# Kernel optimization log

Hardware: AMD Instinct MI355X
Metric: run time of the kernel (lower is better)

Reference implementation:

```python
import jax, jax.numpy as jnp
import numpy as np

S = 4096
DMODEL = 1024
DK = 128

def setup_inputs() -> dict:
    key = jax.random.key(0)
    ks = jax.random.split(key, 7)
    X = jax.random.normal(ks[0], (S, DMODEL), dtype=jnp.float32)
    # nn.Linear(dmodel, dk): weight [dk, dmodel], bias [dk]
    sc = 1.0 / np.sqrt(DMODEL)
    Wq = jax.random.uniform(ks[1], (DK, DMODEL), jnp.float32, -sc, sc)
    bq = jax.random.uniform(ks[2], (DK,), jnp.float32, -sc, sc)
    Wk = jax.random.uniform(ks[3], (DK, DMODEL), jnp.float32, -sc, sc)
    bk = jax.random.uniform(ks[4], (DK,), jnp.float32, -sc, sc)
    Wv = jax.random.uniform(ks[5], (DK, DMODEL), jnp.float32, -sc, sc)
    bv = jax.random.uniform(ks[6], (DK,), jnp.float32, -sc, sc)
    return {"X": X, "Wq": Wq, "bq": bq, "Wk": Wk, "bk": bk, "Wv": Wv, "bv": bv}

def reference(X, Wq, bq, Wk, bk, Wv, bv):
    # QKV projections: [S, dk]
    Q = X @ Wq.T + bq
    K = X @ Wk.T + bk
    V = X @ Wv.T + bv
    scale = 1.0 / jnp.sqrt(jnp.asarray(DK, X.dtype))
    scores = (Q @ K.T) * scale  # [S, S]
    s = X.shape[0]
    causal = jnp.tril(jnp.ones((s, s), dtype=bool))  # True = keep
    scores = jnp.where(causal, scores, -jnp.inf)
    A = jax.nn.softmax(scores, axis=-1)  # dropout p=0 -> identity
    return A @ V  # [S, dk]
```

## Files before the change

### kernel.cpp

```cpp
#include <hip/hip_runtime.h>
#include <hip/hip_bf16.h>

#define S 4096
#define DMODEL 1024
#define DK 128
#define NB_ATTN 2112

typedef __attribute__((ext_vector_type(8))) short  short8;
typedef __attribute__((ext_vector_type(4))) float  f32x4;
typedef __attribute__((ext_vector_type(4))) unsigned short u16x4;

__device__ __forceinline__ unsigned short f2bf(float f) {
    return __builtin_bit_cast(unsigned short, __float2bfloat16(f));
}

__device__ __forceinline__ short8 cvt8(float4 a, float4 b) {
    short8 v;
    v[0] = (short)f2bf(a.x); v[1] = (short)f2bf(a.y);
    v[2] = (short)f2bf(a.z); v[3] = (short)f2bf(a.w);
    v[4] = (short)f2bf(b.x); v[5] = (short)f2bf(b.y);
    v[6] = (short)f2bf(b.z); v[7] = (short)f2bf(b.w);
    return v;
}

__global__ __launch_bounds__(256) void cvt_kernel(
    const float* __restrict__ X,
    const float* __restrict__ Wq, const float* __restrict__ Wk,
    const float* __restrict__ Wv,
    unsigned short* __restrict__ Xb, unsigned short* __restrict__ Wb)
{
    const int i = blockIdx.x * 256 + threadIdx.x;
    const float* __restrict__ src;
    unsigned short* __restrict__ dst;
    size_t off;
    if (i < 524288) {
        src = X; dst = Xb; off = (size_t)i * 8;
    } else {
        const int j   = i - 524288;
        const int sel = j >> 14, jj = j & 16383;
        src = sel == 0 ? Wq : sel == 1 ? Wk : Wv;
        dst = Wb + (size_t)sel * DK * DMODEL;
        off = (size_t)jj * 8;
    }
    const float4 a = *(const float4*)(src + off);
    const float4 b = *(const float4*)(src + off + 4);
    *(short8*)(dst + off) = cvt8(a, b);
}

__global__ __launch_bounds__(128) void proj_gemm(
    const unsigned short* __restrict__ Xb, const unsigned short* __restrict__ Wb,
    const float* __restrict__ bq, const float* __restrict__ bk,
    const float* __restrict__ bv,
    unsigned short* __restrict__ Qb, unsigned short* __restrict__ Kb,
    unsigned short* __restrict__ Vt)
{
    const int sel = blockIdx.y;
    const float* __restrict__ bias = sel == 0 ? bq : sel == 1 ? bk : bv;
    const unsigned short* __restrict__ wbase = Wb + (size_t)sel * DK * DMODEL;

    const int tid = threadIdx.x, w = tid >> 6, lane = tid & 63;
    const int li = lane & 15, gl = lane >> 4;
    const int r0 = blockIdx.x * 16;
    const int n0 = w * 64;

    f32x4 acc[4];
    #pragma unroll
    for (int j = 0; j < 4; ++j)
        #pragma unroll
        for (int r = 0; r < 4; ++r) acc[j][r] = 0.f;

    const unsigned short* ap  = &Xb[(size_t)(r0 + li) * DMODEL + 8 * gl];
    const unsigned short* bp0 = &wbase[(size_t)(n0 + li) * DMODEL + 8 * gl];
    const unsigned short* bp1 = bp0 + (size_t)16 * DMODEL;
    const unsigned short* bp2 = bp0 + (size_t)32 * DMODEL;
    const unsigned short* bp3 = bp0 + (size_t)48 * DMODEL;

    #pragma unroll 4
    for (int k0 = 0; k0 < DMODEL; k0 += 32) {
        const short8 a  = *(const short8*)(ap + k0);
        const short8 b0 = *(const short8*)(bp0 + k0);
        const short8 b1 = *(const short8*)(bp1 + k0);
        const short8 b2 = *(const short8*)(bp2 + k0);
        const short8 b3 = *(const short8*)(bp3 + k0);
        acc[0] = __builtin_amdgcn_mfma_f32_16x16x32_bf16(a, b0, acc[0], 0, 0, 0);
        acc[1] = __builtin_amdgcn_mfma_f32_16x16x32_bf16(a, b1, acc[1], 0, 0, 0);
        acc[2] = __builtin_amdgcn_mfma_f32_16x16x32_bf16(a, b2, acc[2], 0, 0, 0);
        acc[3] = __builtin_amdgcn_mfma_f32_16x16x32_bf16(a, b3, acc[3], 0, 0, 0);
    }

    if (sel < 2) {
        unsigned short* __restrict__ Out = sel == 0 ? Qb : Kb;
        #pragma unroll
        for (int j = 0; j < 4; ++j)
            #pragma unroll
            for (int r = 0; r < 4; ++r) {
                const int row = r0 + 4 * gl + r;
                const int col = n0 + 16 * j + li;
                Out[(size_t)row * DK + col] = f2bf(acc[j][r] + bias[col]);
            }
    } else {
        #pragma unroll
        for (int j = 0; j < 4; ++j) {
            const int col = n0 + 16 * j + li;
            const float bb = bias[col];
            u16x4 wv;
            #pragma unroll
            for (int r = 0; r < 4; ++r) wv[r] = f2bf(acc[j][r] + bb);
            *(u16x4*)&Vt[(size_t)col * S + r0 + 4 * gl] = wv;
        }
    }
}

__global__ __launch_bounds__(64) void attn_mfma(
    const unsigned short* __restrict__ Qb,
    const unsigned short* __restrict__ Kb,
    const unsigned short* __restrict__ Vt,
    float* __restrict__ OP, float* __restrict__ ML)
{
    const int b = (NB_ATTN - 1) - (int)blockIdx.x;
    int j = 1;
    while (2 * (j + 1) * j <= b) ++j;
    const int off = b - 2 * j * (j - 1);
    const int t   = 4 * (j - 1) + off / j;
    const int c   = off % j;
    const int kstart = 128 * c;
    const int kend   = min(128 * (c + 1), 32 * t + 32);

    const int lane = threadIdx.x, li = lane & 15, gl = lane >> 4;

    __shared__ unsigned short Pl[32][40];

    short8 aq[2][4];
    #pragma unroll
    for (int qs = 0; qs < 2; ++qs)
        #pragma unroll
        for (int s = 0; s < 4; ++s)
            aq[qs][s] = *(const short8*)
                &Qb[(size_t)(32 * t + 16 * qs + li) * DK + 32 * s + 8 * gl];

    f32x4 accv[2][8];
    #pragma unroll
    for (int qs = 0; qs < 2; ++qs)
        #pragma unroll
        for (int n = 0; n < 8; ++n)
            #pragma unroll
            for (int r = 0; r < 4; ++r) accv[qs][n][r] = 0.f;

    float mr[2] = {-1e30f, -1e30f}, lr[2] = {0.f, 0.f};
    const float scale = 0.08838834764831845f;

    short8 bkc[2][4], bkn[2][4];
    #pragma unroll
    for (int kt = 0; kt < 2; ++kt)
        #pragma unroll
        for (int s = 0; s < 4; ++s)
            bkc[kt][s] = *(const short8*)
                &Kb[(size_t)(kstart + 16 * kt + li) * DK + 32 * s + 8 * gl];

    for (int kb = kstart; kb < kend; kb += 32) {
        short8 bv[8];
        #pragma unroll
        for (int n = 0; n < 8; ++n)
            bv[n] = *(const short8*)&Vt[(size_t)(16 * n + li) * S + kb + 8 * gl];

        f32x4 sc[2][2];
        #pragma unroll
        for (int qs = 0; qs < 2; ++qs)
            #pragma unroll
            for (int kt = 0; kt < 2; ++kt)
                #pragma unroll
                for (int r = 0; r < 4; ++r) sc[qs][kt][r] = 0.f;
        __builtin_amdgcn_s_setprio(1);
        #pragma unroll
        for (int qs = 0; qs < 2; ++qs)
            #pragma unroll
            for (int kt = 0; kt < 2; ++kt)
                #pragma unroll
                for (int s = 0; s < 4; ++s)
                    sc[qs][kt] = __builtin_amdgcn_mfma_f32_16x16x32_bf16(
                        bkc[kt][s], aq[qs][s], sc[qs][kt], 0, 0, 0);
        __builtin_amdgcn_s_setprio(0);

        const int kn = (kb + 32 < kend) ? kb + 32 : kb;
        #pragma unroll
        for (int kt = 0; kt < 2; ++kt)
            #pragma unroll
            for (int s = 0; s < 4; ++s)
                bkn[kt][s] = *(const short8*)
                    &Kb[(size_t)(kn + 16 * kt + li) * DK + 32 * s + 8 * gl];

        #pragma unroll
        for (int qs = 0; qs < 2; ++qs) {
            const int q = 32 * t + 16 * qs + li;
            #pragma unroll
            for (int kt = 0; kt < 2; ++kt)
                #pragma unroll
                for (int r = 0; r < 4; ++r) {
                    const int key = kb + 16 * kt + 4 * gl + r;
                    sc[qs][kt][r] = (key > q) ? -1e30f : sc[qs][kt][r] * scale;
                }
        }

        float tm[2];
        #pragma unroll
        for (int qs = 0; qs < 2; ++qs) {
            float v = fmaxf(fmaxf(fmaxf(sc[qs][0][0], sc[qs][0][1]),
                                  fmaxf(sc[qs][0][2], sc[qs][0][3])),
                            fmaxf(fmaxf(sc[qs][1][0], sc[qs][1][1]),
                                  fmaxf(sc[qs][1][2], sc[qs][1][3])));
            v = fmaxf(v, __shfl_xor(v, 16));
            v = fmaxf(v, __shfl_xor(v, 32));
            tm[qs] = v;
        }

        const int need = (tm[0] > mr[0] + 6.f) | (tm[1] > mr[1] + 6.f);
        if (__any(need)) {
            float corr[2];
            #pragma unroll
            for (int qs = 0; qs < 2; ++qs) {
                const float mnew = fmaxf(mr[qs], tm[qs]);
                corr[qs] = __expf(mr[qs] - mnew);
                lr[qs] *= corr[qs];
                mr[qs]  = mnew;
            }
            #pragma unroll
            for (int qs = 0; qs < 2; ++qs)
                #pragma unroll
                for (int r = 0; r < 4; ++r) {
                    const float cr = __shfl(corr[qs], 4 * gl + r);
                    #pragma unroll
                    for (int n = 0; n < 8; ++n) accv[qs][n][r] *= cr;
                }
        }

        #pragma unroll
        for (int qs = 0; qs < 2; ++qs) {
            float ps = 0.f;
            #pragma unroll
            for (int kt = 0; kt < 2; ++kt)
                #pragma unroll
                for (int r = 0; r < 4; ++r) {
                    const float p = __expf(sc[qs][kt][r] - mr[qs]);
                    sc[qs][kt][r] = p;
                    ps += p;
                }
            ps += __shfl_xor(ps, 16);
            ps += __shfl_xor(ps, 32);
            lr[qs] += ps;
        }

        #pragma unroll
        for (int qs = 0; qs < 2; ++qs)
            #pragma unroll
            for (int kt = 0; kt < 2; ++kt) {
                u16x4 wv;
                #pragma unroll
                for (int r = 0; r < 4; ++r) wv[r] = f2bf(sc[qs][kt][r]);
                *(u16x4*)&Pl[16 * qs + li][16 * kt + 4 * gl] = wv;
            }
        const short8 pa0 = *(const short8*)&Pl[li][8 * gl];
        const short8 pa1 = *(const short8*)&Pl[16 + li][8 * gl];

        __builtin_amdgcn_s_setprio(1);
        #pragma unroll
        for (int n = 0; n < 8; ++n) {
            accv[0][n] = __builtin_amdgcn_mfma_f32_16x16x32_bf16(pa0, bv[n], accv[0][n], 0, 0, 0);
            accv[1][n] = __builtin_amdgcn_mfma_f32_16x16x32_bf16(pa1, bv[n], accv[1][n], 0, 0, 0);
        }
        __builtin_amdgcn_s_setprio(0);

        #pragma unroll
        for (int kt = 0; kt < 2; ++kt)
            #pragma unroll
            for (int s = 0; s < 4; ++s) bkc[kt][s] = bkn[kt][s];
    }

    #pragma unroll
    for (int qs = 0; qs < 2; ++qs)
        #pragma unroll
        for (int n = 0; n < 8; ++n)
            #pragma unroll
            for (int r = 0; r < 4; ++r)
                OP[((size_t)b * 32 + 16 * qs + 4 * gl + r) * DK + 16 * n + li]
                    = accv[qs][n][r];
    if (gl == 0) {
        #pragma unroll
        for (int qs = 0; qs < 2; ++qs) {
            ML[((size_t)b * 32 + 16 * qs + li) * 2 + 0] = mr[qs];
            ML[((size_t)b * 32 + 16 * qs + li) * 2 + 1] = lr[qs];
        }
    }
}

__global__ __launch_bounds__(DK) void merge_kernel(
    const float* __restrict__ OP, const float* __restrict__ ML,
    float* __restrict__ out)
{
    const int row = blockIdx.x, dv = threadIdx.x;
    const int t  = row >> 5, rl = row & 31;
    const int j  = (t >> 2) + 1;
    const int base = 2 * j * (j - 1) + (t & 3) * j;

    float M = -1e30f;
    for (int c = 0; c < j; ++c)
        M = fmaxf(M, ML[((size_t)(base + c) * 32 + rl) * 2]);
    float L = 0.f, o = 0.f;
    for (int c = 0; c < j; ++c) {
        const float mc = ML[((size_t)(base + c) * 32 + rl) * 2 + 0];
        const float lc = ML[((size_t)(base + c) * 32 + rl) * 2 + 1];
        const float wgt = __expf(mc - M);
        L += lc * wgt;
        o += wgt * OP[((size_t)(base + c) * 32 + rl) * DK + dv];
    }
    out[(size_t)row * DK + dv] = o / L;
}

extern "C" void kernel_launch(void* const* d_in, const int* in_sizes, int n_in,
                              void* d_out, int out_size, void* d_ws, size_t ws_size,
                              hipStream_t stream)
{
    (void)in_sizes; (void)n_in; (void)out_size; (void)ws_size;
    const float* X  = (const float*)d_in[0];
    const float* Wq = (const float*)d_in[1];
    const float* bq = (const float*)d_in[2];
    const float* Wk = (const float*)d_in[3];
    const float* bk = (const float*)d_in[4];
    const float* Wv = (const float*)d_in[5];
    const float* bv = (const float*)d_in[6];
    float* out = (float*)d_out;

    unsigned short* Wb = (unsigned short*)d_ws;
    unsigned short* Qb = Wb + (size_t)3 * DK * DMODEL;
    unsigned short* Kb = Qb + (size_t)S * DK;
    unsigned short* Vt = Kb + (size_t)S * DK;
    unsigned short* Xb = Vt + (size_t)S * DK;
    float* OP = (float*)Xb;
    float* ML = OP + (size_t)NB_ATTN * 32 * DK;

    cvt_kernel<<<2240, 256, 0, stream>>>(X, Wq, Wk, Wv, Xb, Wb);
    proj_gemm<<<dim3(S / 16, 3), 128, 0, stream>>>(
        Xb, Wb, bq, bk, bv, Qb, Kb, Vt);
    attn_mfma<<<NB_ATTN, 64, 0, stream>>>(Qb, Kb, Vt, OP, ML);
    merge_kernel<<<S, DK, 0, stream>>>(OP, ML, out);
}
```

Baseline: 152.3 us.

## Share K/V tiles in LDS across four waves per attention block

Each attention block now holds four waves covering 128 query rows instead of one wave covering 32. The 128-key K and V chunk is staged through double-buffered shared memory so all four waves reuse it, replacing per-wave global loads. The block/chunk mapping changes to a triangular 128x128 tiling, and the merge kernel is updated to match. The projection GEMM is also split across an extra grid dimension for more parallelism, and OP stores/loads become nontemporal. Risks: fewer blocks in the attention grid, more shared memory per block, and wasted masked work on diagonal tiles.

```diff
diff --git a/kernel.cpp b/kernel.cpp
--- a/kernel.cpp
+++ b/kernel.cpp
@@ -4,7 +4,7 @@
 #define S 4096
 #define DMODEL 1024
 #define DK 128
-#define NB_ATTN 2112
+#define NB_ATTN 528
 
 typedef __attribute__((ext_vector_type(8))) short  short8;
 typedef __attribute__((ext_vector_type(4))) float  f32x4;
@@ -61,37 +61,31 @@
     const int tid = threadIdx.x, w = tid >> 6, lane = tid & 63;
     const int li = lane & 15, gl = lane >> 4;
     const int r0 = blockIdx.x * 16;
-    const int n0 = w * 64;
-
-    f32x4 acc[4];
+    const int n0 = blockIdx.z * 64 + w * 32;
+
+    f32x4 acc[2];
     #pragma unroll
-    for (int j = 0; j < 4; ++j)
+    for (int j = 0; j < 2; ++j)
         #pragma unroll
         for (int r = 0; r < 4; ++r) acc[j][r] = 0.f;
 
     const unsigned short* ap  = &Xb[(size_t)(r0 + li) * DMODEL + 8 * gl];
     const unsigned short* bp0 = &wbase[(size_t)(n0 + li) * DMODEL + 8 * gl];
     const unsigned short* bp1 = bp0 + (size_t)16 * DMODEL;
-    const unsigned short* bp2 = bp0 + (size_t)32 * DMODEL;
-    const unsigned short* bp3 = bp0 + (size_t)48 * DMODEL;
 
     #pragma unroll 4
     for (int k0 = 0; k0 < DMODEL; k0 += 32) {
         const short8 a  = *(const short8*)(ap + k0);
         const short8 b0 = *(const short8*)(bp0 + k0);
         const short8 b1 = *(const short8*)(bp1 + k0);
-        const short8 b2 = *(const short8*)(bp2 + k0);
-        const short8 b3 = *(const short8*)(bp3 + k0);
         acc[0] = __builtin_amdgcn_mfma_f32_16x16x32_bf16(a, b0, acc[0], 0, 0, 0);
         acc[1] = __builtin_amdgcn_mfma_f32_16x16x32_bf16(a, b1, acc[1], 0, 0, 0);
-        acc[2] = __builtin_amdgcn_mfma_f32_16x16x32_bf16(a, b2, acc[2], 0, 0, 0);
-        acc[3] = __builtin_amdgcn_mfma_f32_16x16x32_bf16(a, b3, acc[3], 0, 0, 0);
     }
 
     if (sel < 2) {
         unsigned short* __restrict__ Out = sel == 0 ? Qb : Kb;
         #pragma unroll
-        for (int j = 0; j < 4; ++j)
+        for (int j = 0; j < 2; ++j)
             #pragma unroll
             for (int r = 0; r < 4; ++r) {
                 const int row = r0 + 4 * gl + r;
@@ -100,7 +94,7 @@
             }
     } else {
         #pragma unroll
-        for (int j = 0; j < 4; ++j) {
+        for (int j = 0; j < 2; ++j) {
             const int col = n0 + 16 * j + li;
             const float bb = bias[col];
             u16x4 wv;
@@ -111,24 +105,25 @@
     }
 }
 
-__global__ __launch_bounds__(64) void attn_mfma(
+__global__ __launch_bounds__(256, 2) void attn_mfma(
     const unsigned short* __restrict__ Qb,
     const unsigned short* __restrict__ Kb,
     const unsigned short* __restrict__ Vt,
     float* __restrict__ OP, float* __restrict__ ML)
 {
-    const int b = (NB_ATTN - 1) - (int)blockIdx.x;
-    int j = 1;
-    while (2 * (j + 1) * j <= b) ++j;
-    const int off = b - 2 * j * (j - 1);
-    const int t   = 4 * (j - 1) + off / j;
-    const int c   = off % j;
+    const int bb = blockIdx.x;
+    int T = 0;
+    while ((T + 1) * (T + 2) / 2 <= bb) ++T;
+    const int c = bb - T * (T + 1) / 2;
     const int kstart = 128 * c;
-    const int kend   = min(128 * (c + 1), 32 * t + 32);
-
-    const int lane = threadIdx.x, li = lane & 15, gl = lane >> 4;
-
-    __shared__ unsigned short Pl[32][40];
+
+    const int tid = threadIdx.x, w = tid >> 6, lane = tid & 63;
+    const int li = lane & 15, gl = lane >> 4;
+    const int q0 = 128 * T + 32 * w;
+
+    __shared__ unsigned short Ks[2][32 * DK];
+    __shared__ unsigned short Vs[2][DK * 32];
+    __shared__ unsigned short Pl[4][32][40];
 
     short8 aq[2][4];
     #pragma unroll
@@ -136,7 +131,7 @@
         #pragma unroll
         for (int s = 0; s < 4; ++s)
             aq[qs][s] = *(const short8*)
-                &Qb[(size_t)(32 * t + 16 * qs + li) * DK + 32 * s + 8 * gl];
+                &Qb[(size_t)(q0 + 16 * qs + li) * DK + 32 * s + 8 * gl];
 
     f32x4 accv[2][8];
     #pragma unroll
@@ -149,19 +144,43 @@
     float mr[2] = {-1e30f, -1e30f}, lr[2] = {0.f, 0.f};
     const float scale = 0.08838834764831845f;
 
-    short8 bkc[2][4], bkn[2][4];
-    #pragma unroll
-    for (int kt = 0; kt < 2; ++kt)
-        #pragma unroll
-        for (int s = 0; s < 4; ++s)
-            bkc[kt][s] = *(const short8*)
-                &Kb[(size_t)(kstart + 16 * kt + li) * DK + 32 * s + 8 * gl];
-
-    for (int kb = kstart; kb < kend; kb += 32) {
-        short8 bv[8];
+    {
+        short8 st0 = *(const short8*)&Kb[(size_t)(kstart + (tid >> 4)) * DK + (tid & 15) * 8];
+        short8 st1 = *(const short8*)&Kb[(size_t)(kstart + (tid >> 4) + 16) * DK + (tid & 15) * 8];
+        short8 st2 = *(const short8*)&Vt[(size_t)(tid >> 2) * S + kstart + (tid & 3) * 8];
+        short8 st3 = *(const short8*)&Vt[(size_t)((tid >> 2) + 64) * S + kstart + (tid & 3) * 8];
+        *(short8*)&Ks[0][(size_t)tid * 8]         = st0;
+        *(short8*)&Ks[0][(size_t)(tid + 256) * 8] = st1;
+        *(short8*)&Vs[0][(size_t)tid * 8]         = st2;
+        *(short8*)&Vs[0][(size_t)(tid + 256) * 8] = st3;
+    }
+    __syncthreads();
+
+    int cur = 0;
+    for (int it = 0; it < 4; ++it) {
+        const int kb = kstart + 32 * it;
+        const bool pf = (it < 3);
+
+        short8 st0, st1, st2, st3;
+        if (pf) {
+            const int kn = kb + 32;
+            st0 = *(const short8*)&Kb[(size_t)(kn + (tid >> 4)) * DK + (tid & 15) * 8];
+            st1 = *(const short8*)&Kb[(size_t)(kn + (tid >> 4) + 16) * DK + (tid & 15) * 8];
+            st2 = *(const short8*)&Vt[(size_t)(tid >> 2) * S + kn + (tid & 3) * 8];
+            st3 = *(const short8*)&Vt[(size_t)((tid >> 2) + 64) * S + kn + (tid & 3) * 8];
+        }
+
+        const unsigned short* Ksb = &Ks[cur][0];
+        const unsigned short* Vsb = &Vs[cur][0];
+        short8 kf[2][4], vf[8];
+        #pragma unroll
+        for (int kt = 0; kt < 2; ++kt)
+            #pragma unroll
+            for (int s = 0; s < 4; ++s)
+                kf[kt][s] = *(const short8*)&Ksb[(16 * kt + li) * DK + 32 * s + 8 * gl];
         #pragma unroll
         for (int n = 0; n < 8; ++n)
-            bv[n] = *(const short8*)&Vt[(size_t)(16 * n + li) * S + kb + 8 * gl];
+            vf[n] = *(const short8*)&Vsb[(16 * n + li) * 32 + 8 * gl];
 
         f32x4 sc[2][2];
         #pragma unroll
@@ -178,20 +197,12 @@
                 #pragma unroll
                 for (int s = 0; s < 4; ++s)
                     sc[qs][kt] = __builtin_amdgcn_mfma_f32_16x16x32_bf16(
-                        bkc[kt][s], aq[qs][s], sc[qs][kt], 0, 0, 0);
+                        kf[kt][s], aq[qs][s], sc[qs][kt], 0, 0, 0);
         __builtin_amdgcn_s_setprio(0);
 
-        const int kn = (kb + 32 < kend) ? kb + 32 : kb;
-        #pragma unroll
-        for (int kt = 0; kt < 2; ++kt)
-            #pragma unroll
-            for (int s = 0; s < 4; ++s)
-                bkn[kt][s] = *(const short8*)
-                    &Kb[(size_t)(kn + 16 * kt + li) * DK + 32 * s + 8 * gl];
-
         #pragma unroll
         for (int qs = 0; qs < 2; ++qs) {
-            const int q = 32 * t + 16 * qs + li;
+            const int q = q0 + 16 * qs + li;
             #pragma unroll
             for (int kt = 0; kt < 2; ++kt)
                 #pragma unroll
@@ -256,23 +267,27 @@
                 u16x4 wv;
                 #pragma unroll
                 for (int r = 0; r < 4; ++r) wv[r] = f2bf(sc[qs][kt][r]);
-                *(u16x4*)&Pl[16 * qs + li][16 * kt + 4 * gl] = wv;
+                *(u16x4*)&Pl[w][16 * qs + li][16 * kt + 4 * gl] = wv;
             }
-        const short8 pa0 = *(const short8*)&Pl[li][8 * gl];
-        const short8 pa1 = *(const short8*)&Pl[16 + li][8 * gl];
+        const short8 pa0 = *(const short8*)&Pl[w][li][8 * gl];
+        const short8 pa1 = *(const short8*)&Pl[w][16 + li][8 * gl];
 
         __builtin_amdgcn_s_setprio(1);
         #pragma unroll
         for (int n = 0; n < 8; ++n) {
-            accv[0][n] = __builtin_amdgcn_mfma_f32_16x16x32_bf16(pa0, bv[n], accv[0][n], 0, 0, 0);
-            accv[1][n] = __builtin_amdgcn_mfma_f32_16x16x32_bf16(pa1, bv[n], accv[1][n], 0, 0, 0);
+            accv[0][n] = __builtin_amdgcn_mfma_f32_16x16x32_bf16(pa0, vf[n], accv[0][n], 0, 0, 0);
+            accv[1][n] = __builtin_amdgcn_mfma_f32_16x16x32_bf16(pa1, vf[n], accv[1][n], 0, 0, 0);
         }
         __builtin_amdgcn_s_setprio(0);
 
-        #pragma unroll
-        for (int kt = 0; kt < 2; ++kt)
-            #pragma unroll
-            for (int s = 0; s < 4; ++s) bkc[kt][s] = bkn[kt][s];
+        if (pf) {
+            *(short8*)&Ks[cur ^ 1][(size_t)tid * 8]         = st0;
+            *(short8*)&Ks[cur ^ 1][(size_t)(tid + 256) * 8] = st1;
+            *(short8*)&Vs[cur ^ 1][(size_t)tid * 8]         = st2;
+            *(short8*)&Vs[cur ^ 1][(size_t)(tid + 256) * 8] = st3;
+            __syncthreads();
+        }
+        cur ^= 1;
     }
 
     #pragma unroll
@@ -281,13 +296,14 @@
         for (int n = 0; n < 8; ++n)
             #pragma unroll
             for (int r = 0; r < 4; ++r)
-                OP[((size_t)b * 32 + 16 * qs + 4 * gl + r) * DK + 16 * n + li]
-                    = accv[qs][n][r];
+                __builtin_nontemporal_store(accv[qs][n][r],
+                    &OP[((size_t)bb * 128 + 32 * w + 16 * qs + 4 * gl + r) * DK
+                        + 16 * n + li]);
     if (gl == 0) {
         #pragma unroll
         for (int qs = 0; qs < 2; ++qs) {
-            ML[((size_t)b * 32 + 16 * qs + li) * 2 + 0] = mr[qs];
-            ML[((size_t)b * 32 + 16 * qs + li) * 2 + 1] = lr[qs];
+            ML[((size_t)bb * 128 + 32 * w + 16 * qs + li) * 2 + 0] = mr[qs];
+            ML[((size_t)bb * 128 + 32 * w + 16 * qs + li) * 2 + 1] = lr[qs];
         }
     }
 }
@@ -297,20 +313,22 @@
     float* __restrict__ out)
 {
     const int row = blockIdx.x, dv = threadIdx.x;
-    const int t  = row >> 5, rl = row & 31;
-    const int j  = (t >> 2) + 1;
-    const int base = 2 * j * (j - 1) + (t & 3) * j;
+    const int T  = row >> 7, rl = row & 127;
+    const int j  = T + 1;
+    const int base = T * (T + 1) / 2;
 
     float M = -1e30f;
     for (int c = 0; c < j; ++c)
-        M = fmaxf(M, ML[((size_t)(base + c) * 32 + rl) * 2]);
+        M = fmaxf(M, ML[((size_t)(base + c) * 128 + rl) * 2]);
     float L = 0.f, o = 0.f;
+    #pragma unroll 2
     for (int c = 0; c < j; ++c) {
-        const float mc = ML[((size_t)(base + c) * 32 + rl) * 2 + 0];
-        const float lc = ML[((size_t)(base + c) * 32 + rl) * 2 + 1];
+        const float mc = ML[((size_t)(base + c) * 128 + rl) * 2 + 0];
+        const float lc = ML[((size_t)(base + c) * 128 + rl) * 2 + 1];
         const float wgt = __expf(mc - M);
         L += lc * wgt;
-        o += wgt * OP[((size_t)(base + c) * 32 + rl) * DK + dv];
+        o += wgt * __builtin_nontemporal_load(
+                 &OP[((size_t)(base + c) * 128 + rl) * DK + dv]);
     }
     out[(size_t)row * DK + dv] = o / L;
 }
@@ -335,11 +353,11 @@
     unsigned short* Vt = Kb + (size_t)S * DK;
     unsigned short* Xb = Vt + (size_t)S * DK;
     float* OP = (float*)Xb;
-    float* ML = OP + (size_t)NB_ATTN * 32 * DK;
+    float* ML = OP + (size_t)NB_ATTN * 128 * DK;
 
     cvt_kernel<<<2240, 256, 0, stream>>>(X, Wq, Wk, Wv, Xb, Wb);
-    proj_gemm<<<dim3(S / 16, 3), 128, 0, stream>>>(
+    proj_gemm<<<dim3(S / 16, 3, 2), 128, 0, stream>>>(
         Xb, Wb, bq, bk, bv, Qb, Kb, Vt);
-    attn_mfma<<<NB_ATTN, 64, 0, stream>>>(Qb, Kb, Vt, OP, ML);
+    attn_mfma<<<NB_ATTN, 256, 0, stream>>>(Qb, Kb, Vt, OP, ML);
     merge_kernel<<<S, DK, 0, stream>>>(OP, ML, out);
 }
```

Result: faster. 147.0 us (-3.5%).
